# Optimization experiments

Measured on AMD Instinct MI355X. Metric: run time of the kernel, lower is better.

The kernel has to match this reference:

```python
import jax, jax.numpy as jnp
import numpy as np

WINDOW = 7
TOKEN_SELF_ATTN_VALUE = -5e4  # lucidrains shared-qk self-token score


def _look_around(t, pad_value, w):
    # backward=1, forward=0: pad one window at the front of the window axis,
    # then concat [previous window, current window] along the intra-window axis.
    pad = [(0, 0), (1, 0)] + [(0, 0)] * (t.ndim - 2)
    p = jnp.pad(t, pad, constant_values=pad_value)
    return jnp.concatenate([p[:, :w], p[:, 1:w + 1]], axis=2)


def local_attention(q, k, v, window_size):
    b, n, e = q.shape
    w = n // window_size
    # shared_qk: L2-normalize k (F.normalize, eps=1e-12)
    k = k / jnp.clip(jnp.linalg.norm(k, axis=-1, keepdims=True), 1e-12)
    k = k.astype(q.dtype)

    bq = q.reshape(b, w, window_size, e)
    bk = _look_around(k.reshape(b, w, window_size, e), -1.0, w)   # [b,w,2*ws,e]
    bv = _look_around(v.reshape(b, w, window_size, e), -1.0, w)

    t_idx = jnp.arange(n, dtype=jnp.int32).reshape(1, w, window_size)
    bq_t = t_idx                                   # [1,w,ws]
    bq_k = _look_around(t_idx, -1, w)              # [1,w,2*ws]

    dots = jnp.einsum('bwie,bwje->bwij', bq, bk) * (e ** -0.5)
    mask_value = -jnp.finfo(dots.dtype).max

    self_mask = bq_t[:, :, :, None] == bq_k[:, :, None, :]
    dots = jnp.where(self_mask, TOKEN_SELF_ATTN_VALUE, dots)
    causal_mask = bq_t[:, :, :, None] < bq_k[:, :, None, :]
    dots = jnp.where(causal_mask, mask_value, dots)
    pad_mask = bq_k[:, :, None, :] == -1
    dots = jnp.where(pad_mask, mask_value, dots)

    attn = jax.nn.softmax(dots, axis=-1)
    out = jnp.einsum('bwij,bwje->bwie', attn, bv)
    return out.reshape(b, n, e)


def setup_inputs() -> dict:
    key = jax.random.key(0)
    ks = jax.random.split(key, 7)
    B, H, W, C = 16, 56, 56, 512
    x = jax.random.normal(ks[0], (B, H, W, C), dtype=jnp.float32)
    s = 0.02
    wq = jax.random.normal(ks[1], (C, C), dtype=jnp.float32) * s
    wk = jax.random.normal(ks[2], (C, C), dtype=jnp.float32) * s
    wv = jax.random.normal(ks[3], (C, C), dtype=jnp.float32) * s
    bq = jax.random.normal(ks[4], (C,), dtype=jnp.float32) * s
    bk = jax.random.normal(ks[5], (C,), dtype=jnp.float32) * s
    bv = jax.random.normal(ks[6], (C,), dtype=jnp.float32) * s
    return {"x": x, "wq": wq, "bq": bq, "wk": wk, "bk": bk, "wv": wv, "bv": bv}


def reference(x, wq, bq, wk, bk, wv, bv):
    b, h, w, c = x.shape
    xf = x.reshape(b, h * w, c)
    q = xf @ wq + bq
    k = xf @ wk + bk
    v = xf @ wv + bv
    out = local_attention(q, k, v, WINDOW)
    return out.reshape(b, h, w, c)
```

## Files before the change

### kernel.cpp

```cpp
#include <hip/hip_runtime.h>
#include <math.h>

#define NTOK_PER_B 3136
#define NBATCH 16
#define M_TOK (NTOK_PER_B * NBATCH)
#define CDIM 512
#define NWIN 448
#define SCALE 0.04419417382415922f

typedef _Float16 half8 __attribute__((ext_vector_type(8)));
typedef float f32x4 __attribute__((ext_vector_type(4)));

#define GLOAD16(g, l) __builtin_amdgcn_global_load_lds( \
    (const __attribute__((address_space(1))) void*)(g),  \
    (__attribute__((address_space(3))) void*)(l), 16, 0, 0)

__device__ __forceinline__ float wave_sum64(float s) {
    #pragma unroll
    for (int o = 32; o >= 1; o >>= 1) s += __shfl_xor(s, o, 64);
    return s;
}

__global__ __launch_bounds__(256) void cvt_f32_f16(
    const float* __restrict__ x, _Float16* __restrict__ y)
{
    const size_t i = ((size_t)blockIdx.x * 256 + threadIdx.x) * 8;
    const float4 a = *(const float4*)(x + i);
    const float4 b = *(const float4*)(x + i + 4);
    half8 o;
    o[0] = (_Float16)a.x; o[1] = (_Float16)a.y; o[2] = (_Float16)a.z; o[3] = (_Float16)a.w;
    o[4] = (_Float16)b.x; o[5] = (_Float16)b.y; o[6] = (_Float16)b.z; o[7] = (_Float16)b.w;
    *(half8*)(y + i) = o;
}

__global__ __launch_bounds__(256) void cvt_w_t(
    const float* __restrict__ w0, const float* __restrict__ w1,
    const float* __restrict__ w2, _Float16* __restrict__ wt)
{
    const float* w = (blockIdx.z == 0) ? w0 : ((blockIdx.z == 1) ? w1 : w2);
    _Float16* o = wt + (size_t)blockIdx.z * CDIM * CDIM;
    __shared__ float tile[32][33];
    const int tx = threadIdx.x & 31;
    const int ty = threadIdx.x >> 5;
    const int k0 = blockIdx.x * 32;
    const int n0 = blockIdx.y * 32;
    #pragma unroll
    for (int r = 0; r < 32; r += 8)
        tile[ty + r][tx] = w[(size_t)(k0 + ty + r) * CDIM + n0 + tx];
    __syncthreads();
    #pragma unroll
    for (int r = 0; r < 32; r += 8)
        o[(size_t)(n0 + ty + r) * CDIM + k0 + tx] = (_Float16)tile[tx][ty + r];
}

__global__ __launch_bounds__(256) void qkv_gemm_f16(
    const _Float16* __restrict__ A,
    const _Float16* __restrict__ Wt,
    const float* __restrict__ b0, const float* __restrict__ b1,
    const float* __restrict__ b2,
    _Float16* __restrict__ out)
{
    const int z = blockIdx.z;
    const _Float16* W = Wt + (size_t)z * CDIM * CDIM;
    const float* bias = (z == 0) ? b0 : ((z == 1) ? b1 : b2);
    _Float16* O = out + (size_t)z * (size_t)M_TOK * CDIM;

    __shared__ _Float16 As[128 * 32];
    __shared__ _Float16 Bs[128 * 32];

    const int t    = threadIdx.x;
    const int lane = t & 63;
    const int wid  = t >> 6;
    const int wrow = (wid >> 1) * 64;
    const int wcol = (wid & 1) * 64;
    const int row0 = blockIdx.x * 128;
    const int col0 = blockIdx.y * 128;

    const _Float16* aSrc0 = A + (size_t)(row0 + (t >> 2)) * CDIM + (t & 3) * 8;
    const _Float16* aSrc1 = aSrc0 + (size_t)64 * CDIM;
    const _Float16* bSrc0 = W + (size_t)(col0 + (t >> 2)) * CDIM + (t & 3) * 8;
    const _Float16* bSrc1 = bSrc0 + (size_t)64 * CDIM;
    _Float16* aDst0 = As + t * 8;
    _Float16* aDst1 = As + (t + 256) * 8;
    _Float16* bDst0 = Bs + t * 8;
    _Float16* bDst1 = Bs + (t + 256) * 8;

    f32x4 acc[4][4];
    #pragma unroll
    for (int m = 0; m < 4; ++m)
        #pragma unroll
        for (int n = 0; n < 4; ++n)
            acc[m][n] = (f32x4){0.f, 0.f, 0.f, 0.f};

    const int fr  = lane & 15;
    const int q8o = (lane >> 4) * 8;

    for (int k0 = 0; k0 < CDIM; k0 += 32) {
        GLOAD16(aSrc0 + k0, aDst0);
        GLOAD16(aSrc1 + k0, aDst1);
        GLOAD16(bSrc0 + k0, bDst0);
        GLOAD16(bSrc1 + k0, bDst1);
        __syncthreads();

        half8 af[4], bf[4];
        #pragma unroll
        for (int m = 0; m < 4; ++m)
            af[m] = *(const half8*)(As + (wrow + m * 16 + fr) * 32 + q8o);
        #pragma unroll
        for (int n = 0; n < 4; ++n)
            bf[n] = *(const half8*)(Bs + (wcol + n * 16 + fr) * 32 + q8o);
        #pragma unroll
        for (int m = 0; m < 4; ++m)
            #pragma unroll
            for (int n = 0; n < 4; ++n)
                acc[m][n] = __builtin_amdgcn_mfma_f32_16x16x32_f16(
                    af[m], bf[n], acc[m][n], 0, 0, 0);
        __syncthreads();
    }

    const int rq = (lane >> 4) * 4;
    float bval[4];
    #pragma unroll
    for (int n = 0; n < 4; ++n)
        bval[n] = bias[col0 + wcol + n * 16 + fr];
    #pragma unroll
    for (int m = 0; m < 4; ++m) {
        #pragma unroll
        for (int r = 0; r < 4; ++r) {
            const int row = row0 + wrow + m * 16 + rq + r;
            _Float16* op = O + (size_t)row * CDIM + col0 + wcol + fr;
            #pragma unroll
            for (int n = 0; n < 4; ++n)
                op[n * 16] = (_Float16)(acc[m][n][r] + bval[n]);
        }
    }
}

__global__ __launch_bounds__(256) void knorm_f16(_Float16* __restrict__ k)
{
    const int tok  = blockIdx.x * 4 + (threadIdx.x >> 6);
    const int lane = threadIdx.x & 63;
    _Float16* p = k + (size_t)tok * CDIM + lane * 8;
    half8 v = *(const half8*)p;
    float s = 0.f;
    #pragma unroll
    for (int e = 0; e < 8; ++e) {
        const float f = (float)v[e];
        s = fmaf(f, f, s);
    }
    s = wave_sum64(s);
    const float scale = 1.f / fmaxf(sqrtf(s), 1e-12f);
    #pragma unroll
    for (int e = 0; e < 8; ++e)
        v[e] = (_Float16)((float)v[e] * scale);
    *(half8*)p = v;
}

__global__ __launch_bounds__(448) void local_attn_f16(
    const _Float16* __restrict__ q,
    const _Float16* __restrict__ k,
    const _Float16* __restrict__ v,
    float* __restrict__ out)
{
    const int blk   = blockIdx.x;
    const int batch = blk / NWIN;
    const int win   = blk % NWIN;
    const int i     = threadIdx.x >> 6;
    const int lane  = threadIdx.x & 63;
    const int c     = lane * 8;

    const long long tok0 = (long long)batch * NTOK_PER_B + (long long)win * 7;

    const half8 q8 = *(const half8*)(q + (tok0 + i) * CDIM + c);

    float dots[14];
    #pragma unroll
    for (int j = 0; j < 14; ++j) {
        const bool valid = (win > 0) || (j >= 7);
        float d = 0.f;
        if (valid) {
            const half8 k8 = *(const half8*)(k + (tok0 - 7 + j) * CDIM + c);
            #pragma unroll
            for (int e = 0; e < 8; ++e)
                d = fmaf((float)q8[e], (float)k8[e], d);
        }
        dots[j] = wave_sum64(d);
    }

    float sc[14];
    #pragma unroll
    for (int j = 0; j < 14; ++j) {
        const bool valid = (win > 0) || (j >= 7);
        if (j > i + 7 || !valid)  sc[j] = -3.402823466e38f;
        else if (j == i + 7)      sc[j] = -5e4f;
        else                      sc[j] = dots[j] * SCALE;
    }
    float m = sc[0];
    #pragma unroll
    for (int j = 1; j < 14; ++j) m = fmaxf(m, sc[j]);
    float sum = 0.f;
    #pragma unroll
    for (int j = 0; j < 14; ++j) {
        sc[j] = __expf(sc[j] - m);
        sum += sc[j];
    }
    const float inv = 1.f / sum;

    float o[8];
    #pragma unroll
    for (int e = 0; e < 8; ++e) o[e] = 0.f;
    #pragma unroll
    for (int j = 0; j < 14; ++j) {
        const bool valid = (win > 0) || (j >= 7);
        if (valid) {
            const half8 v8 = *(const half8*)(v + (tok0 - 7 + j) * CDIM + c);
            const float a = sc[j] * inv;
            #pragma unroll
            for (int e = 0; e < 8; ++e)
                o[e] = fmaf(a, (float)v8[e], o[e]);
        }
    }

    float* op = out + (tok0 + i) * CDIM + c;
    *(float4*)(op)     = make_float4(o[0], o[1], o[2], o[3]);
    *(float4*)(op + 4) = make_float4(o[4], o[5], o[6], o[7]);
}

extern "C" void kernel_launch(void* const* d_in, const int* in_sizes, int n_in,
                              void* d_out, int out_size, void* d_ws, size_t ws_size,
                              hipStream_t stream)
{
    const float* x  = (const float*)d_in[0];
    const float* wq = (const float*)d_in[1];
    const float* bq = (const float*)d_in[2];
    const float* wk = (const float*)d_in[3];
    const float* bk = (const float*)d_in[4];
    const float* wv = (const float*)d_in[5];
    const float* bv = (const float*)d_in[6];
    float* out = (float*)d_out;

    char* ws = (char*)d_ws;
    const size_t XH_BYTES = (size_t)M_TOK * CDIM * sizeof(_Float16);
    const size_t WT_BYTES = (size_t)3 * CDIM * CDIM * sizeof(_Float16);
    _Float16* xh  = (_Float16*)ws;
    _Float16* wt  = (_Float16*)(ws + XH_BYTES);
    _Float16* qkv = (_Float16*)(ws + XH_BYTES + WT_BYTES);
    _Float16* qh = qkv;
    _Float16* kh = qkv + (size_t)M_TOK * CDIM;
    _Float16* vh = kh  + (size_t)M_TOK * CDIM;

    cvt_f32_f16<<<12544, 256, 0, stream>>>(x, xh);
    cvt_w_t<<<dim3(16, 16, 3), 256, 0, stream>>>(wq, wk, wv, wt);
    qkv_gemm_f16<<<dim3(M_TOK / 128, CDIM / 128, 3), 256, 0, stream>>>(
        xh, wt, bq, bk, bv, qkv);
    knorm_f16<<<M_TOK / 4, 256, 0, stream>>>(kh);
    local_attn_f16<<<NBATCH * NWIN, 448, 0, stream>>>(qh, kh, vh, out);
}
```

Measured before the change: 405.1 us.

## Fuse Q/K/V GEMMs into one kernel and fold K-normalization into attention

The GEMM now computes all three projections in one block, so each A tile is loaded once and reused for three weight tiles, with triple accumulators. The separate K-normalization kernel is removed. K row norms are instead computed inside the attention kernel from K values already held in registers and applied as a divisor on the dot products. The 48 accumulator tiles per thread greatly raise register pressure and lower occupancy. K is now stored unnormalized in fp16, which changes rounding slightly.

```diff
diff --git a/kernel.cpp b/kernel.cpp
--- a/kernel.cpp
+++ b/kernel.cpp
@@ -53,20 +53,15 @@
         o[(size_t)(n0 + ty + r) * CDIM + k0 + tx] = (_Float16)tile[tx][ty + r];
 }
 
-__global__ __launch_bounds__(256) void qkv_gemm_f16(
+__global__ __launch_bounds__(256) void qkv_gemm_f16_fused(
     const _Float16* __restrict__ A,
     const _Float16* __restrict__ Wt,
     const float* __restrict__ b0, const float* __restrict__ b1,
     const float* __restrict__ b2,
     _Float16* __restrict__ out)
 {
-    const int z = blockIdx.z;
-    const _Float16* W = Wt + (size_t)z * CDIM * CDIM;
-    const float* bias = (z == 0) ? b0 : ((z == 1) ? b1 : b2);
-    _Float16* O = out + (size_t)z * (size_t)M_TOK * CDIM;
-
     __shared__ _Float16 As[128 * 32];
-    __shared__ _Float16 Bs[128 * 32];
+    __shared__ _Float16 Bs[3][128 * 32];
 
     const int t    = threadIdx.x;
     const int lane = t & 63;
@@ -78,19 +73,18 @@
 
     const _Float16* aSrc0 = A + (size_t)(row0 + (t >> 2)) * CDIM + (t & 3) * 8;
     const _Float16* aSrc1 = aSrc0 + (size_t)64 * CDIM;
-    const _Float16* bSrc0 = W + (size_t)(col0 + (t >> 2)) * CDIM + (t & 3) * 8;
-    const _Float16* bSrc1 = bSrc0 + (size_t)64 * CDIM;
+    const size_t bRow = (size_t)(col0 + (t >> 2)) * CDIM + (t & 3) * 8;
     _Float16* aDst0 = As + t * 8;
     _Float16* aDst1 = As + (t + 256) * 8;
-    _Float16* bDst0 = Bs + t * 8;
-    _Float16* bDst1 = Bs + (t + 256) * 8;
-
-    f32x4 acc[4][4];
-    #pragma unroll
-    for (int m = 0; m < 4; ++m)
-        #pragma unroll
-        for (int n = 0; n < 4; ++n)
-            acc[m][n] = (f32x4){0.f, 0.f, 0.f, 0.f};
+
+    f32x4 acc[3][4][4];
+    #pragma unroll
+    for (int z = 0; z < 3; ++z)
+        #pragma unroll
+        for (int m = 0; m < 4; ++m)
+            #pragma unroll
+            for (int n = 0; n < 4; ++n)
+                acc[z][m][n] = (f32x4){0.f, 0.f, 0.f, 0.f};
 
     const int fr  = lane & 15;
     const int q8o = (lane >> 4) * 8;
@@ -98,62 +92,55 @@
     for (int k0 = 0; k0 < CDIM; k0 += 32) {
         GLOAD16(aSrc0 + k0, aDst0);
         GLOAD16(aSrc1 + k0, aDst1);
-        GLOAD16(bSrc0 + k0, bDst0);
-        GLOAD16(bSrc1 + k0, bDst1);
+        #pragma unroll
+        for (int z = 0; z < 3; ++z) {
+            const _Float16* bs = Wt + (size_t)z * CDIM * CDIM + bRow + k0;
+            GLOAD16(bs, &Bs[z][t * 8]);
+            GLOAD16(bs + (size_t)64 * CDIM, &Bs[z][(t + 256) * 8]);
+        }
         __syncthreads();
 
-        half8 af[4], bf[4];
+        half8 af[4];
         #pragma unroll
         for (int m = 0; m < 4; ++m)
             af[m] = *(const half8*)(As + (wrow + m * 16 + fr) * 32 + q8o);
         #pragma unroll
+        for (int z = 0; z < 3; ++z) {
+            half8 bf[4];
+            #pragma unroll
+            for (int n = 0; n < 4; ++n)
+                bf[n] = *(const half8*)(&Bs[z][0] + (wcol + n * 16 + fr) * 32 + q8o);
+            #pragma unroll
+            for (int m = 0; m < 4; ++m)
+                #pragma unroll
+                for (int n = 0; n < 4; ++n)
+                    acc[z][m][n] = __builtin_amdgcn_mfma_f32_16x16x32_f16(
+                        af[m], bf[n], acc[z][m][n], 0, 0, 0);
+        }
+        __syncthreads();
+    }
+
+    const int rq = (lane >> 4) * 4;
+    #pragma unroll
+    for (int z = 0; z < 3; ++z) {
+        const float* bias = (z == 0) ? b0 : ((z == 1) ? b1 : b2);
+        _Float16* O = out + (size_t)z * (size_t)M_TOK * CDIM;
+        float bval[4];
+        #pragma unroll
         for (int n = 0; n < 4; ++n)
-            bf[n] = *(const half8*)(Bs + (wcol + n * 16 + fr) * 32 + q8o);
-        #pragma unroll
-        for (int m = 0; m < 4; ++m)
-            #pragma unroll
-            for (int n = 0; n < 4; ++n)
-                acc[m][n] = __builtin_amdgcn_mfma_f32_16x16x32_f16(
-                    af[m], bf[n], acc[m][n], 0, 0, 0);
-        __syncthreads();
-    }
-
-    const int rq = (lane >> 4) * 4;
-    float bval[4];
-    #pragma unroll
-    for (int n = 0; n < 4; ++n)
-        bval[n] = bias[col0 + wcol + n * 16 + fr];
-    #pragma unroll
-    for (int m = 0; m < 4; ++m) {
-        #pragma unroll
-        for (int r = 0; r < 4; ++r) {
-            const int row = row0 + wrow + m * 16 + rq + r;
-            _Float16* op = O + (size_t)row * CDIM + col0 + wcol + fr;
-            #pragma unroll
-            for (int n = 0; n < 4; ++n)
-                op[n * 16] = (_Float16)(acc[m][n][r] + bval[n]);
-        }
-    }
-}
-
-__global__ __launch_bounds__(256) void knorm_f16(_Float16* __restrict__ k)
-{
-    const int tok  = blockIdx.x * 4 + (threadIdx.x >> 6);
-    const int lane = threadIdx.x & 63;
-    _Float16* p = k + (size_t)tok * CDIM + lane * 8;
-    half8 v = *(const half8*)p;
-    float s = 0.f;
-    #pragma unroll
-    for (int e = 0; e < 8; ++e) {
-        const float f = (float)v[e];
-        s = fmaf(f, f, s);
-    }
-    s = wave_sum64(s);
-    const float scale = 1.f / fmaxf(sqrtf(s), 1e-12f);
-    #pragma unroll
-    for (int e = 0; e < 8; ++e)
-        v[e] = (_Float16)((float)v[e] * scale);
-    *(half8*)p = v;
+            bval[n] = bias[col0 + wcol + n * 16 + fr];
+        #pragma unroll
+        for (int m = 0; m < 4; ++m) {
+            #pragma unroll
+            for (int r = 0; r < 4; ++r) {
+                const int row = row0 + wrow + m * 16 + rq + r;
+                _Float16* op = O + (size_t)row * CDIM + col0 + wcol + fr;
+                #pragma unroll
+                for (int n = 0; n < 4; ++n)
+                    op[n * 16] = (_Float16)(acc[z][m][n][r] + bval[n]);
+            }
+        }
+    }
 }
 
 __global__ __launch_bounds__(448) void local_attn_f16(
@@ -169,23 +156,54 @@
     const int lane  = threadIdx.x & 63;
     const int c     = lane * 8;
 
+    __shared__ float norms_s[14];
+
     const long long tok0 = (long long)batch * NTOK_PER_B + (long long)win * 7;
 
     const half8 q8 = *(const half8*)(q + (tok0 + i) * CDIM + c);
 
+    half8 kreg[14];
+    #pragma unroll
+    for (int j = 0; j < 14; ++j) {
+        const bool valid = (win > 0) || (j >= 7);
+        if (valid) kreg[j] = *(const half8*)(k + (tok0 - 7 + j) * CDIM + c);
+        else       kreg[j] = (half8)(_Float16)0.f;
+    }
+
+    float np[14];
+    #pragma unroll
+    for (int j = 0; j < 14; ++j) {
+        float s = 0.f;
+        #pragma unroll
+        for (int e = 0; e < 8; ++e) {
+            const float f = (float)kreg[j][e];
+            s = fmaf(f, f, s);
+        }
+        np[j] = s;
+    }
+    float na = 0.f, nb = 0.f;
+    #pragma unroll
+    for (int j = 0; j < 14; ++j) {
+        if (j == 2 * i)     na = np[j];
+        if (j == 2 * i + 1) nb = np[j];
+    }
+    na = wave_sum64(na);
+    nb = wave_sum64(nb);
+    if (lane == 0) {
+        norms_s[2 * i]     = sqrtf(na);
+        norms_s[2 * i + 1] = sqrtf(nb);
+    }
+
     float dots[14];
     #pragma unroll
     for (int j = 0; j < 14; ++j) {
-        const bool valid = (win > 0) || (j >= 7);
         float d = 0.f;
-        if (valid) {
-            const half8 k8 = *(const half8*)(k + (tok0 - 7 + j) * CDIM + c);
-            #pragma unroll
-            for (int e = 0; e < 8; ++e)
-                d = fmaf((float)q8[e], (float)k8[e], d);
-        }
+        #pragma unroll
+        for (int e = 0; e < 8; ++e)
+            d = fmaf((float)q8[e], (float)kreg[j][e], d);
         dots[j] = wave_sum64(d);
     }
+    __syncthreads();
 
     float sc[14];
     #pragma unroll
@@ -193,7 +211,7 @@
         const bool valid = (win > 0) || (j >= 7);
         if (j > i + 7 || !valid)  sc[j] = -3.402823466e38f;
         else if (j == i + 7)      sc[j] = -5e4f;
-        else                      sc[j] = dots[j] * SCALE;
+        else                      sc[j] = dots[j] * SCALE / fmaxf(norms_s[j], 1e-12f);
     }
     float m = sc[0];
     #pragma unroll
@@ -251,8 +269,7 @@
 
     cvt_f32_f16<<<12544, 256, 0, stream>>>(x, xh);
     cvt_w_t<<<dim3(16, 16, 3), 256, 0, stream>>>(wq, wk, wv, wt);
-    qkv_gemm_f16<<<dim3(M_TOK / 128, CDIM / 128, 3), 256, 0, stream>>>(
+    qkv_gemm_f16_fused<<<dim3(M_TOK / 128, CDIM / 128), 256, 0, stream>>>(
         xh, wt, bq, bk, bv, qkv);
-    knorm_f16<<<M_TOK / 4, 256, 0, stream>>>(kh);
     local_attn_f16<<<NBATCH * NWIN, 448, 0, stream>>>(qh, kh, vh, out);
 }
```

Result: slower. 581.7 us (+43.6%).

## Double-buffer QKV GEMM LDS tiles and swap grid order for A-tile reuse

Applied to the files above, without the earlier changes.

The QKV projection GEMM now keeps two LDS buffers. It issues global_load_lds for the next k-slice before the MFMA work on the current slice, so one barrier per iteration replaces two and load latency overlaps compute. The grid is also transposed so that consecutive blocks share the same 128-row A tile across the four column tiles, which should improve L2 reuse of the large activation matrix. LDS use doubles to 32KB per block, which may lower occupancy. A possible correctness concern is that the async LDS writes for the next stage are not explicitly waited on before the barrier.

```diff
diff --git a/kernel.cpp b/kernel.cpp
--- a/kernel.cpp
+++ b/kernel.cpp
@@ -65,25 +65,21 @@
     const float* bias = (z == 0) ? b0 : ((z == 1) ? b1 : b2);
     _Float16* O = out + (size_t)z * (size_t)M_TOK * CDIM;
 
-    __shared__ _Float16 As[128 * 32];
-    __shared__ _Float16 Bs[128 * 32];
+    __shared__ _Float16 As[2][128 * 32];
+    __shared__ _Float16 Bs[2][128 * 32];
 
     const int t    = threadIdx.x;
     const int lane = t & 63;
     const int wid  = t >> 6;
     const int wrow = (wid >> 1) * 64;
     const int wcol = (wid & 1) * 64;
-    const int row0 = blockIdx.x * 128;
-    const int col0 = blockIdx.y * 128;
+    const int row0 = blockIdx.y * 128;
+    const int col0 = blockIdx.x * 128;
 
     const _Float16* aSrc0 = A + (size_t)(row0 + (t >> 2)) * CDIM + (t & 3) * 8;
     const _Float16* aSrc1 = aSrc0 + (size_t)64 * CDIM;
     const _Float16* bSrc0 = W + (size_t)(col0 + (t >> 2)) * CDIM + (t & 3) * 8;
     const _Float16* bSrc1 = bSrc0 + (size_t)64 * CDIM;
-    _Float16* aDst0 = As + t * 8;
-    _Float16* aDst1 = As + (t + 256) * 8;
-    _Float16* bDst0 = Bs + t * 8;
-    _Float16* bDst1 = Bs + (t + 256) * 8;
 
     f32x4 acc[4][4];
     #pragma unroll
@@ -95,28 +91,43 @@
     const int fr  = lane & 15;
     const int q8o = (lane >> 4) * 8;
 
-    for (int k0 = 0; k0 < CDIM; k0 += 32) {
-        GLOAD16(aSrc0 + k0, aDst0);
-        GLOAD16(aSrc1 + k0, aDst1);
-        GLOAD16(bSrc0 + k0, bDst0);
-        GLOAD16(bSrc1 + k0, bDst1);
+#define STAGE(buf, kofs)                                          \
+    do {                                                          \
+        GLOAD16(aSrc0 + (kofs), &As[buf][t * 8]);                 \
+        GLOAD16(aSrc1 + (kofs), &As[buf][(t + 256) * 8]);         \
+        GLOAD16(bSrc0 + (kofs), &Bs[buf][t * 8]);                 \
+        GLOAD16(bSrc1 + (kofs), &Bs[buf][(t + 256) * 8]);         \
+    } while (0)
+
+#define COMPUTE(buf)                                                        \
+    do {                                                                    \
+        half8 af[4], bf[4];                                                 \
+        _Pragma("unroll")                                                   \
+        for (int m = 0; m < 4; ++m)                                         \
+            af[m] = *(const half8*)(&As[buf][(wrow + m * 16 + fr) * 32 + q8o]); \
+        _Pragma("unroll")                                                   \
+        for (int n = 0; n < 4; ++n)                                         \
+            bf[n] = *(const half8*)(&Bs[buf][(wcol + n * 16 + fr) * 32 + q8o]); \
+        _Pragma("unroll")                                                   \
+        for (int m = 0; m < 4; ++m)                                         \
+            _Pragma("unroll")                                               \
+            for (int n = 0; n < 4; ++n)                                     \
+                acc[m][n] = __builtin_amdgcn_mfma_f32_16x16x32_f16(         \
+                    af[m], bf[n], acc[m][n], 0, 0, 0);                      \
+    } while (0)
+
+    STAGE(0, 0);
+    __syncthreads();
+
+    int cur = 0;
+    #pragma unroll 1
+    for (int ks = 0; ks < 15; ++ks) {
+        STAGE(cur ^ 1, (ks + 1) * 32);
+        COMPUTE(cur);
         __syncthreads();
-
-        half8 af[4], bf[4];
-        #pragma unroll
-        for (int m = 0; m < 4; ++m)
-            af[m] = *(const half8*)(As + (wrow + m * 16 + fr) * 32 + q8o);
-        #pragma unroll
-        for (int n = 0; n < 4; ++n)
-            bf[n] = *(const half8*)(Bs + (wcol + n * 16 + fr) * 32 + q8o);
-        #pragma unroll
-        for (int m = 0; m < 4; ++m)
-            #pragma unroll
-            for (int n = 0; n < 4; ++n)
-                acc[m][n] = __builtin_amdgcn_mfma_f32_16x16x32_f16(
-                    af[m], bf[n], acc[m][n], 0, 0, 0);
-        __syncthreads();
-    }
+        cur ^= 1;
+    }
+    COMPUTE(cur);
 
     const int rq = (lane >> 4) * 4;
     float bval[4];
@@ -134,6 +145,8 @@
                 op[n * 16] = (_Float16)(acc[m][n][r] + bval[n]);
         }
     }
+#undef STAGE
+#undef COMPUTE
 }
 
 __global__ __launch_bounds__(256) void knorm_f16(_Float16* __restrict__ k)
@@ -251,7 +264,7 @@
 
     cvt_f32_f16<<<12544, 256, 0, stream>>>(x, xh);
     cvt_w_t<<<dim3(16, 16, 3), 256, 0, stream>>>(wq, wk, wv, wt);
-    qkv_gemm_f16<<<dim3(M_TOK / 128, CDIM / 128, 3), 256, 0, stream>>>(
+    qkv_gemm_f16<<<dim3(CDIM / 128, M_TOK / 128, 3), 256, 0, stream>>>(
         xh, wt, bq, bk, bv, qkv);
     knorm_f16<<<M_TOK / 4, 256, 0, stream>>>(kh);
     local_attn_f16<<<NBATCH * NWIN, 448, 0, stream>>>(qh, kh, vh, out);
```

New measurement: 409.2 us. No clear change (+1.0%).

## Map one wave per attention window and loop over its seven query rows

Applied to the files above, without the earlier changes.

The local attention kernel now gives each 64-lane wave a whole window and iterates over its seven query rows, with four windows per 256-thread block, instead of one block per window with one wave per query. The per-window boundary branches on K/V loads are removed, and the 14 wave reductions are batched after all partial dot products. The aim is to let each wave reuse the window's K/V rows across queries and to cut launch and branch overhead. In exchange there is much less thread-level parallelism and a serial per-wave loop. Window 0 of batch 0 now reads seven rows before the K and V buffers; those scores are masked out, but the reads touch neighbouring workspace memory.

```diff
diff --git a/kernel.cpp b/kernel.cpp
--- a/kernel.cpp
+++ b/kernel.cpp
@@ -156,74 +156,75 @@
     *(half8*)p = v;
 }
 
-__global__ __launch_bounds__(448) void local_attn_f16(
+__global__ __launch_bounds__(256) void local_attn_f16(
     const _Float16* __restrict__ q,
     const _Float16* __restrict__ k,
     const _Float16* __restrict__ v,
     float* __restrict__ out)
 {
-    const int blk   = blockIdx.x;
-    const int batch = blk / NWIN;
-    const int win   = blk % NWIN;
-    const int i     = threadIdx.x >> 6;
+    const int wave  = threadIdx.x >> 6;
     const int lane  = threadIdx.x & 63;
+    const int gwin  = blockIdx.x * 4 + wave;
+    const int batch = gwin / NWIN;
+    const int win   = gwin % NWIN;
     const int c     = lane * 8;
 
     const long long tok0 = (long long)batch * NTOK_PER_B + (long long)win * 7;
-
-    const half8 q8 = *(const half8*)(q + (tok0 + i) * CDIM + c);
-
-    float dots[14];
-    #pragma unroll
-    for (int j = 0; j < 14; ++j) {
-        const bool valid = (win > 0) || (j >= 7);
-        float d = 0.f;
-        if (valid) {
-            const half8 k8 = *(const half8*)(k + (tok0 - 7 + j) * CDIM + c);
+    const _Float16* kbase = k + (tok0 - 7) * CDIM + c;
+    const _Float16* vbase = v + (tok0 - 7) * CDIM + c;
+    const bool w0 = (win == 0);
+
+    for (int i = 0; i < 7; ++i) {
+        const half8 q8 = *(const half8*)(q + (tok0 + i) * CDIM + c);
+
+        float dots[14];
+        #pragma unroll
+        for (int j = 0; j < 14; ++j) {
+            const half8 k8 = *(const half8*)(kbase + j * CDIM);
+            float d = 0.f;
             #pragma unroll
             for (int e = 0; e < 8; ++e)
                 d = fmaf((float)q8[e], (float)k8[e], d);
-        }
-        dots[j] = wave_sum64(d);
-    }
-
-    float sc[14];
-    #pragma unroll
-    for (int j = 0; j < 14; ++j) {
-        const bool valid = (win > 0) || (j >= 7);
-        if (j > i + 7 || !valid)  sc[j] = -3.402823466e38f;
-        else if (j == i + 7)      sc[j] = -5e4f;
-        else                      sc[j] = dots[j] * SCALE;
-    }
-    float m = sc[0];
-    #pragma unroll
-    for (int j = 1; j < 14; ++j) m = fmaxf(m, sc[j]);
-    float sum = 0.f;
-    #pragma unroll
-    for (int j = 0; j < 14; ++j) {
-        sc[j] = __expf(sc[j] - m);
-        sum += sc[j];
-    }
-    const float inv = 1.f / sum;
-
-    float o[8];
-    #pragma unroll
-    for (int e = 0; e < 8; ++e) o[e] = 0.f;
-    #pragma unroll
-    for (int j = 0; j < 14; ++j) {
-        const bool valid = (win > 0) || (j >= 7);
-        if (valid) {
-            const half8 v8 = *(const half8*)(v + (tok0 - 7 + j) * CDIM + c);
+            dots[j] = d;
+        }
+        #pragma unroll
+        for (int j = 0; j < 14; ++j)
+            dots[j] = wave_sum64(dots[j]);
+
+        float sc[14];
+        #pragma unroll
+        for (int j = 0; j < 14; ++j) {
+            if (j > i + 7 || (w0 && j < 7)) sc[j] = -3.402823466e38f;
+            else if (j == i + 7)            sc[j] = -5e4f;
+            else                            sc[j] = dots[j] * SCALE;
+        }
+        float m = sc[0];
+        #pragma unroll
+        for (int j = 1; j < 14; ++j) m = fmaxf(m, sc[j]);
+        float sum = 0.f;
+        #pragma unroll
+        for (int j = 0; j < 14; ++j) {
+            sc[j] = __expf(sc[j] - m);
+            sum += sc[j];
+        }
+        const float inv = 1.f / sum;
+
+        float o[8];
+        #pragma unroll
+        for (int e = 0; e < 8; ++e) o[e] = 0.f;
+        #pragma unroll
+        for (int j = 0; j < 14; ++j) {
+            const half8 v8 = *(const half8*)(vbase + j * CDIM);
             const float a = sc[j] * inv;
             #pragma unroll
             for (int e = 0; e < 8; ++e)
                 o[e] = fmaf(a, (float)v8[e], o[e]);
         }
-    }
-
-    float* op = out + (tok0 + i) * CDIM + c;
-    *(float4*)(op)     = make_float4(o[0], o[1], o[2], o[3]);
-    *(float4*)(op + 4) = make_float4(o[4], o[5], o[6], o[7]);
+
+        float* op = out + (tok0 + i) * CDIM + c;
+        *(float4*)(op)     = make_float4(o[0], o[1], o[2], o[3]);
+        *(float4*)(op + 4) = make_float4(o[4], o[5], o[6], o[7]);
+    }
 }
 
 extern "C" void kernel_launch(void* const* d_in, const int* in_sizes, int n_in,
@@ -254,5 +255,5 @@
     qkv_gemm_f16<<<dim3(M_TOK / 128, CDIM / 128, 3), 256, 0, stream>>>(
         xh, wt, bq, bk, bv, qkv);
     knorm_f16<<<M_TOK / 4, 256, 0, stream>>>(kh);
-    local_attn_f16<<<NBATCH * NWIN, 448, 0, stream>>>(qh, kh, vh, out);
-}
+    local_attn_f16<<<(NBATCH * NWIN) / 4, 256, 0, stream>>>(qh, kh, vh, out);
+}
```

Measured after the change: 494.3 us. 1.22x slower.
